# Kernel tuning notes

Measured on AMD Instinct MI355X. Metric: run time of the kernel, lower is better.

Reference implementation:

```python
import jax, jax.numpy as jnp
import numpy as np

B, S, D = 16, 8192, 512
H, K, V = 8, 64, 64
EPS = 1e-12  # tf.math.l2_normalize epsilon


def setup_inputs() -> dict:
    key = jax.random.key(0)
    ks = jax.random.split(key, 12)
    s = 0.02
    return {
        "x": jax.random.normal(ks[0], (B, S, D), jnp.float32),
        "mask": jnp.ones((B, S), dtype=bool),
        "Wq_r": jax.random.normal(ks[1], (H, D, K), jnp.float32) * s,
        "bq_r": jnp.zeros((H, K), jnp.float32),
        "Wq_i": jax.random.normal(ks[2], (H, D, K), jnp.float32) * s,
        "bq_i": jnp.zeros((H, K), jnp.float32),
        "Wv": jax.random.normal(ks[3], (H, D, V), jnp.float32) * s,
        "bv": jnp.zeros((H, V), jnp.float32),
        "key_real": jax.random.normal(ks[4], (H, K), jnp.float32),
        "key_imag": jax.random.normal(ks[5], (H, K), jnp.float32),
        "Wf": jax.random.normal(ks[6], (H * V, D), jnp.float32) * s,
        "bf": jnp.zeros((D,), jnp.float32),
    }


def reference(x, mask, Wq_r, bq_r, Wq_i, bq_i, Wv, bv, key_real, key_imag, Wf, bf):
    m = mask.astype(x.dtype)  # [B,S]
    # all heads' query (complex: real/imag) and value projections in batched GEMMs
    qr = jnp.einsum('bsd,hdk->bshk', x, Wq_r) + bq_r  # [B,S,H,K]
    qi = jnp.einsum('bsd,hdk->bshk', x, Wq_i) + bq_i
    v = jnp.einsum('bsd,hdv->bshv', x, Wv) + bv       # [B,S,H,V]
    # complex l2_normalize along last axis: z / sqrt(sum |z|^2)
    qn = jnp.sqrt(jnp.maximum(jnp.sum(qr * qr + qi * qi, -1, keepdims=True), EPS))
    qr, qi = qr / qn, qi / qn
    kn = jnp.sqrt(jnp.maximum(jnp.sum(key_real**2 + key_imag**2, -1, keepdims=True), EPS))
    kr, ki = key_real / kn, key_imag / kn             # [H,K]
    # real part of non-conjugated complex dot product (operation='real')
    score = jnp.einsum('bshk,hk->bsh', qr, kr) - jnp.einsum('bshk,hk->bsh', qi, ki)
    score = score * m[:, :, None]                     # [B,S,H]
    pooled = jnp.einsum('bsh,bshv->bhv', score, v)    # masked weighted sum over S
    res = pooled.reshape(pooled.shape[0], -1)          # concat heads -> [B,H*V]
    return res @ Wf + bf                               # feedforward -> [B,D]
```

## Files before the change

kernel.cpp:

```cpp
#include <hip/hip_runtime.h>
#include <hip/hip_bf16.h>


#define CB 16
#define CS 8192
#define CD 512
#define CH 8
#define CK 64
#define NCOL 128
#define TM 64
#define EPSV 1e-12f

typedef __attribute__((ext_vector_type(8))) unsigned short us8;
typedef __attribute__((ext_vector_type(8))) __bf16 bf16x8;
typedef __attribute__((ext_vector_type(4))) float f32x4;

__device__ __forceinline__ unsigned short f2bf(float f) {
  __hip_bfloat16 h = __float2bfloat16(f);
  return *reinterpret_cast<unsigned short*>(&h);
}
__device__ __forceinline__ float bf2f(unsigned short u) {
  unsigned int x = ((unsigned int)u) << 16;
  return __uint_as_float(x);
}
__device__ __forceinline__ bf16x8 as_bf(us8 u) { return __builtin_bit_cast(bf16x8, u); }

#define G2L16(gp, lp)                                                  \
  __builtin_amdgcn_global_load_lds(                                    \
      (const __attribute__((address_space(1))) unsigned int*)(gp),     \
      (__attribute__((address_space(3))) unsigned int*)(lp), 16, 0, 0)

__global__ void cap_prep(const float* __restrict__ Wq_r, const float* __restrict__ Wq_i,
                         unsigned short* __restrict__ wbt) {
  __shared__ float tile[64][65];
  int blk = blockIdx.x, t = threadIdx.x;
  int ri = blk >> 6, h = (blk >> 3) & 7, dt = blk & 7;
  const float* src = (ri ? Wq_i : Wq_r) + (size_t)h * CD * CK + (size_t)dt * 64 * CK;
  #pragma unroll
  for (int p = 0; p < 16; ++p) {
    int idx = p * 256 + t;
    int d = idx >> 6, c = idx & 63;
    tile[d][c] = src[(size_t)d * CK + c];
  }
  __syncthreads();
  int l = t & 63;
  #pragma unroll
  for (int p = 0; p < 16; ++p) {
    int c = p * 4 + (t >> 6);
    wbt[((size_t)(h * NCOL + ri * 64 + c)) * CD + dt * 64 + l] = f2bf(tile[l][c]);
  }
}

__global__ void cap_keys(const float* __restrict__ key_real, const float* __restrict__ key_imag,
                         const float* __restrict__ bq_r, const float* __restrict__ bq_i,
                         float* __restrict__ wvec, float* __restrict__ bqc) {
  int h = blockIdx.x, t = threadIdx.x;
  __shared__ float kn;
  if (t < 64) {
    float a = key_real[h * CK + t], b2 = key_imag[h * CK + t];
    float s = a * a + b2 * b2;
    #pragma unroll
    for (int off = 1; off < 64; off <<= 1) s += __shfl_xor(s, off);
    if (t == 0) kn = sqrtf(fmaxf(s, EPSV));
  }
  __syncthreads();
  float v = (t < CK) ? key_real[h * CK + t] : -key_imag[h * CK + (t - CK)];
  wvec[h * NCOL + t] = v / kn;
  bqc[h * NCOL + t] = (t < CK) ? bq_r[h * CK + t] : bq_i[h * CK + (t - CK)];
}

#define XL_BYTES 65536
#define WBUF_BYTES 32768
#define SMEM_BYTES (XL_BYTES + 2 * WBUF_BYTES + 3 * 2048)

__global__ __launch_bounds__(512, 2) void cap_main(
    const float* __restrict__ x, const int* __restrict__ mask,
    const unsigned short* __restrict__ wbt, const float* __restrict__ wvec,
    const float* __restrict__ bqc, float* __restrict__ yws, float* __restrict__ ssum) {
  extern __shared__ char smem[];
  char* Xl = smem;
  char* Wb = smem + XL_BYTES;
  float* partn = (float*)(smem + XL_BYTES + 2 * WBUF_BYTES);
  float* partm = partn + 512;
  float* scoresA = partm + 512;

  const int tid = threadIdx.x;
  const int w = tid >> 6, l = tid & 63;
  const int lr = l & 15, q = l >> 4;
  const int b = blockIdx.x >> 7;
  const int s0 = (blockIdx.x & 127) * TM;
  const float* xrow = x + ((size_t)(b * CS + s0)) * CD;

  auto stageW = [&](int s) {
    if (s >= 32) return;
    int ch = s >> 4, kc = s & 15;
    char* dst = Wb + (size_t)(s & 1) * WBUF_BYTES;
    #pragma unroll
    for (int i = 0; i < 4; ++i) {
      int o = i * 8192 + tid * 16;
      int col_local = o >> 6;
      int kchunk = (o >> 4) & 3;
      const unsigned short* src =
          wbt + ((size_t)(ch * 512 + col_local)) * CD + kc * 32 + kchunk * 8;
      G2L16(src, dst + o);
    }
  };

  stageW(0);

  #pragma unroll
  for (int i = 0; i < 8; ++i) {
    int id = i * 512 + tid;
    int row = id >> 6, cc = id & 63;
    const float* src = xrow + row * CD + cc * 8;
    float4 f0 = *(const float4*)(src);
    float4 f1 = *(const float4*)(src + 4);
    us8 v;
    v[0] = f2bf(f0.x); v[1] = f2bf(f0.y); v[2] = f2bf(f0.z); v[3] = f2bf(f0.w);
    v[4] = f2bf(f1.x); v[5] = f2bf(f1.y); v[6] = f2bf(f1.z); v[7] = f2bf(f1.w);
    int byte = row * 1024 + ((cc * 16) ^ ((row & 7) << 4));
    *(us8*)(Xl + byte) = v;
  }
  __syncthreads();

  #pragma unroll 1
  for (int ch = 0; ch < 2; ++ch) {
    f32x4 acc[4][4];
    #pragma unroll
    for (int m = 0; m < 4; ++m)
      #pragma unroll
      for (int n = 0; n < 4; ++n) acc[m][n] = (f32x4){0.f, 0.f, 0.f, 0.f};

    #pragma unroll 1
    for (int kc = 0; kc < 16; ++kc) {
      int gp = ch * 16 + kc;
      stageW(gp + 1);
      char* wl = Wb + (size_t)(gp & 1) * WBUF_BYTES;
      int kbyte = kc * 64 + q * 16;
      bf16x8 a[4], bb[4];
      #pragma unroll
      for (int m = 0; m < 4; ++m) {
        int row = m * 16 + lr;
        a[m] = as_bf(*(const us8*)(Xl + row * 1024 + (kbyte ^ ((row & 7) << 4))));
      }
      #pragma unroll
      for (int n = 0; n < 4; ++n) {
        int col_local = w * 64 + n * 16 + lr;
        bb[n] = as_bf(*(const us8*)(wl + col_local * 64 + q * 16));
      }
      #pragma unroll
      for (int m = 0; m < 4; ++m)
        #pragma unroll
        for (int n = 0; n < 4; ++n)
          acc[m][n] = __builtin_amdgcn_mfma_f32_16x16x32_bf16(a[m], bb[n], acc[m][n], 0, 0, 0);
      __syncthreads();
    }

    {
      int h = ch * 4 + (w >> 1);
      float n2[4][4], nm[4][4];
      #pragma unroll
      for (int m = 0; m < 4; ++m)
        #pragma unroll
        for (int r = 0; r < 4; ++r) { n2[m][r] = 0.f; nm[m][r] = 0.f; }
      #pragma unroll
      for (int n = 0; n < 4; ++n) {
        int c = (w & 1) * 64 + n * 16 + lr;
        float wv = wvec[h * NCOL + c];
        float bq = bqc[h * NCOL + c];
        #pragma unroll
        for (int m = 0; m < 4; ++m)
          #pragma unroll
          for (int r = 0; r < 4; ++r) {
            float qv = acc[m][n][r] + bq;
            n2[m][r] += qv * qv;
            nm[m][r] += qv * wv;
          }
      }
      #pragma unroll
      for (int off = 1; off < 16; off <<= 1)
        #pragma unroll
        for (int m = 0; m < 4; ++m)
          #pragma unroll
          for (int r = 0; r < 4; ++r) {
            n2[m][r] += __shfl_xor(n2[m][r], off);
            nm[m][r] += __shfl_xor(nm[m][r], off);
          }
      if (lr == 0) {
        #pragma unroll
        for (int m = 0; m < 4; ++m)
          #pragma unroll
          for (int r = 0; r < 4; ++r) {
            int row = m * 16 + q * 4 + r;
            partn[w * 64 + row] = n2[m][r];
            partm[w * 64 + row] = nm[m][r];
          }
      }
      __syncthreads();
      if (tid < 64) {
        float mk = (mask[(size_t)b * CS + s0 + tid] != 0) ? 1.0f : 0.0f;
        #pragma unroll
        for (int hl = 0; hl < 4; ++hl) {
          float nn = partn[(2 * hl) * 64 + tid] + partn[(2 * hl + 1) * 64 + tid];
          float mm = partm[(2 * hl) * 64 + tid] + partm[(2 * hl + 1) * 64 + tid];
          float sc = mm / sqrtf(fmaxf(nn, EPSV)) * mk;
          scoresA[(ch * 4 + hl) * 64 + tid] = sc;
          float ts = sc;
          #pragma unroll
          for (int off = 1; off < 64; off <<= 1) ts += __shfl_xor(ts, off);
          if (tid == 0) atomicAdd(&ssum[b * CH + ch * 4 + hl], ts);
        }
      }
      __syncthreads();
    }
  }

  {
    int d = tid;
    float sreg[CH];
    #pragma unroll
    for (int h = 0; h < CH; ++h) sreg[h] = scoresA[h * 64 + l];
    float yacc[CH];
    #pragma unroll
    for (int h = 0; h < CH; ++h) yacc[h] = 0.f;
    #pragma unroll 4
    for (int row = 0; row < TM; ++row) {
      int byte = row * 1024 + ((d * 2) ^ ((row & 7) << 4));
      float xv = bf2f(*(const unsigned short*)(Xl + byte));
      #pragma unroll
      for (int h = 0; h < CH; ++h) {
        float sc = __uint_as_float(
            __builtin_amdgcn_readlane(__float_as_uint(sreg[h]), row));
        yacc[h] += sc * xv;
      }
    }
    #pragma unroll
    for (int h = 0; h < CH; ++h)
      atomicAdd(&yws[((size_t)b * CH + h) * CD + d], yacc[h]);
  }
}

__global__ void cap_pooled(const float* __restrict__ yws, const float* __restrict__ ssum,
                           const float* __restrict__ Wv, const float* __restrict__ bv,
                           float* __restrict__ pooled) {
  int blk = blockIdx.x, t = threadIdx.x;
  int b = blk >> 3, h = blk & 7;
  int v = t & 63, dq = t >> 6;
  const float* y = yws + ((size_t)b * CH + h) * CD;
  const float* wv = Wv + (size_t)h * CD * CK;
  float acc = 0.f;
  #pragma unroll 8
  for (int i = 0; i < 128; ++i) {
    int d = i * 4 + dq;
    acc += y[d] * wv[(size_t)d * CK + v];
  }
  __shared__ float red[4][64];
  red[dq][v] = acc;
  __syncthreads();
  if (t < 64) {
    float s = red[0][t] + red[1][t] + red[2][t] + red[3][t] +
              ssum[b * CH + h] * bv[h * CK + t];
    pooled[(size_t)b * 512 + h * 64 + t] = s;
  }
}

__global__ void cap_out(const float* __restrict__ pooled, const float* __restrict__ Wf,
                        const float* __restrict__ bfv, float* __restrict__ out) {
  int blk = blockIdx.x, t = threadIdx.x;
  int b = blk >> 3, dc = blk & 7;
  int dl = t & 63, jq = t >> 6;
  int dout = dc * 64 + dl;
  const float* pr = pooled + (size_t)b * 512;
  float acc = 0.f;
  #pragma unroll 8
  for (int i = 0; i < 128; ++i) {
    int j = i * 4 + jq;
    acc += pr[j] * Wf[(size_t)j * CD + dout];
  }
  __shared__ float red[4][64];
  red[jq][dl] = acc;
  __syncthreads();
  if (t < 64)
    out[(size_t)b * CD + dc * 64 + t] =
        red[0][t] + red[1][t] + red[2][t] + red[3][t] + bfv[dc * 64 + t];
}

extern "C" void kernel_launch(void* const* d_in, const int* in_sizes, int n_in,
                              void* d_out, int out_size, void* d_ws, size_t ws_size,
                              hipStream_t stream) {
  const float* x = (const float*)d_in[0];
  const int* mask = (const int*)d_in[1];
  const float* Wq_r = (const float*)d_in[2];
  const float* bq_r = (const float*)d_in[3];
  const float* Wq_i = (const float*)d_in[4];
  const float* bq_i = (const float*)d_in[5];
  const float* Wv = (const float*)d_in[6];
  const float* bv = (const float*)d_in[7];
  const float* key_real = (const float*)d_in[8];
  const float* key_imag = (const float*)d_in[9];
  const float* Wf = (const float*)d_in[10];
  const float* bfv = (const float*)d_in[11];
  float* out = (float*)d_out;

  char* ws = (char*)d_ws;
  unsigned short* wbt = (unsigned short*)ws;
  float* wvec = (float*)(ws + (1 << 20));
  float* bqc  = (float*)(ws + (1 << 20) + 4096);
  float* yws  = (float*)(ws + (1 << 20) + 8192);
  float* ssum = (float*)(ws + (1 << 20) + 8192 + CB * CH * CD * 4);
  float* pooled = (float*)(ws + (1 << 20) + 8192 + CB * CH * CD * 4 + 512);

  hipMemsetAsync(yws, 0, CB * CH * CD * 4 + CB * CH * 4, stream);
  cap_prep<<<dim3(128), dim3(256), 0, stream>>>(Wq_r, Wq_i, wbt);
  cap_keys<<<dim3(8), dim3(128), 0, stream>>>(key_real, key_imag, bq_r, bq_i, wvec, bqc);
  hipFuncSetAttribute((const void*)cap_main,
                      hipFuncAttributeMaxDynamicSharedMemorySize, SMEM_BYTES);
  cap_main<<<dim3(CB * (CS / TM)), dim3(512), SMEM_BYTES, stream>>>(
      x, mask, wbt, wvec, bqc, yws, ssum);
  cap_pooled<<<dim3(128), dim3(256), 0, stream>>>(yws, ssum, Wv, bv, pooled);
  cap_out<<<dim3(128), dim3(256), 0, stream>>>(pooled, Wf, bfv, out);
}
```

Measured before the change: 735.1 us.

## Make main kernel persistent over tiles with register-streamed weights and fused epilogue

Each block of the main kernel now processes eight consecutive 64-row tiles instead of one, and the grid shrinks from 2048 to 256 blocks. Weight fragments are loaded straight from global memory into double-buffered registers instead of being staged through LDS. The next tile of x is prefetched into registers during the last k-chunk. Per-tile score-sum atomics and y atomics are accumulated in registers and flushed once per block, and the 16-lane reductions use DPP row rotates. The two tail kernels are merged into a single per-batch finish kernel. The changes aim to cut LDS staging, per-k barriers, atomics and launches, at the cost of higher register pressure, more global weight traffic through L2, and only 256 blocks to spread across the GPU.

```diff
diff --git a/kernel.cpp b/kernel.cpp
--- a/kernel.cpp
+++ b/kernel.cpp
@@ -9,6 +9,7 @@
 #define CK 64
 #define NCOL 128
 #define TM 64
+#define NT 8
 #define EPSV 1e-12f
 
 typedef __attribute__((ext_vector_type(8))) unsigned short us8;
@@ -25,10 +26,18 @@
 }
 __device__ __forceinline__ bf16x8 as_bf(us8 u) { return __builtin_bit_cast(bf16x8, u); }
 
-#define G2L16(gp, lp)                                                  \
-  __builtin_amdgcn_global_load_lds(                                    \
-      (const __attribute__((address_space(1))) unsigned int*)(gp),     \
-      (__attribute__((address_space(3))) unsigned int*)(lp), 16, 0, 0)
+__device__ __forceinline__ float ror_add16(float v) {
+  int x;
+  x = __builtin_amdgcn_update_dpp(0, __float_as_int(v), 0x128, 0xf, 0xf, false);
+  v += __int_as_float(x);
+  x = __builtin_amdgcn_update_dpp(0, __float_as_int(v), 0x124, 0xf, 0xf, false);
+  v += __int_as_float(x);
+  x = __builtin_amdgcn_update_dpp(0, __float_as_int(v), 0x122, 0xf, 0xf, false);
+  v += __int_as_float(x);
+  x = __builtin_amdgcn_update_dpp(0, __float_as_int(v), 0x121, 0xf, 0xf, false);
+  v += __int_as_float(x);
+  return v;
+}
 
 __global__ void cap_prep(const float* __restrict__ Wq_r, const float* __restrict__ Wq_i,
                          unsigned short* __restrict__ wbt) {
@@ -70,8 +79,7 @@
 }
 
 #define XL_BYTES 65536
-#define WBUF_BYTES 32768
-#define SMEM_BYTES (XL_BYTES + 2 * WBUF_BYTES + 3 * 2048)
+#define SMEM_BYTES (XL_BYTES + 3 * 512 * 4)
 
 __global__ __launch_bounds__(512, 2) void cap_main(
     const float* __restrict__ x, const int* __restrict__ mask,
@@ -79,113 +87,124 @@
     const float* __restrict__ bqc, float* __restrict__ yws, float* __restrict__ ssum) {
   extern __shared__ char smem[];
   char* Xl = smem;
-  char* Wb = smem + XL_BYTES;
-  float* partn = (float*)(smem + XL_BYTES + 2 * WBUF_BYTES);
+  float* scoresA = (float*)(smem + XL_BYTES);
+  float* partn = scoresA + 512;
   float* partm = partn + 512;
-  float* scoresA = partm + 512;
 
   const int tid = threadIdx.x;
   const int w = tid >> 6, l = tid & 63;
   const int lr = l & 15, q = l >> 4;
-  const int b = blockIdx.x >> 7;
-  const int s0 = (blockIdx.x & 127) * TM;
-  const float* xrow = x + ((size_t)(b * CS + s0)) * CD;
-
-  auto stageW = [&](int s) {
-    if (s >= 32) return;
-    int ch = s >> 4, kc = s & 15;
-    char* dst = Wb + (size_t)(s & 1) * WBUF_BYTES;
-    #pragma unroll
-    for (int i = 0; i < 4; ++i) {
-      int o = i * 8192 + tid * 16;
-      int col_local = o >> 6;
-      int kchunk = (o >> 4) & 3;
-      const unsigned short* src =
-          wbt + ((size_t)(ch * 512 + col_local)) * CD + kc * 32 + kchunk * 8;
-      G2L16(src, dst + o);
-    }
-  };
-
-  stageW(0);
+  const int b = blockIdx.x >> 4;
+  const int s_base = (blockIdx.x & 15) * (NT * TM);
+  const float* xbase = x + ((size_t)b * CS + s_base) * CD;
+  const us8* wbt8 = (const us8*)wbt;
+  const int hw = w >> 1, chalf = w & 1;
+
+  float yacc[CH], ssacc[CH];
+  #pragma unroll
+  for (int h = 0; h < CH; ++h) { yacc[h] = 0.f; ssacc[h] = 0.f; }
+
+  float4 xp[16];
 
   #pragma unroll
   for (int i = 0; i < 8; ++i) {
     int id = i * 512 + tid;
     int row = id >> 6, cc = id & 63;
-    const float* src = xrow + row * CD + cc * 8;
-    float4 f0 = *(const float4*)(src);
-    float4 f1 = *(const float4*)(src + 4);
+    const float* src = xbase + row * CD + cc * 8;
+    xp[i * 2] = *(const float4*)(src);
+    xp[i * 2 + 1] = *(const float4*)(src + 4);
+  }
+  #pragma unroll
+  for (int i = 0; i < 8; ++i) {
+    int id = i * 512 + tid;
+    int row = id >> 6, cc = id & 63;
+    float4 f0 = xp[i * 2], f1 = xp[i * 2 + 1];
     us8 v;
     v[0] = f2bf(f0.x); v[1] = f2bf(f0.y); v[2] = f2bf(f0.z); v[3] = f2bf(f0.w);
     v[4] = f2bf(f1.x); v[5] = f2bf(f1.y); v[6] = f2bf(f1.z); v[7] = f2bf(f1.w);
-    int byte = row * 1024 + ((cc * 16) ^ ((row & 7) << 4));
-    *(us8*)(Xl + byte) = v;
+    *(us8*)(Xl + row * 1024 + ((cc * 16) ^ ((row & 7) << 4))) = v;
   }
   __syncthreads();
 
   #pragma unroll 1
-  for (int ch = 0; ch < 2; ++ch) {
-    f32x4 acc[4][4];
+  for (int t = 0; t < NT; ++t) {
     #pragma unroll
-    for (int m = 0; m < 4; ++m)
-      #pragma unroll
-      for (int n = 0; n < 4; ++n) acc[m][n] = (f32x4){0.f, 0.f, 0.f, 0.f};
-
-    #pragma unroll 1
-    for (int kc = 0; kc < 16; ++kc) {
-      int gp = ch * 16 + kc;
-      stageW(gp + 1);
-      char* wl = Wb + (size_t)(gp & 1) * WBUF_BYTES;
-      int kbyte = kc * 64 + q * 16;
-      bf16x8 a[4], bb[4];
-      #pragma unroll
-      for (int m = 0; m < 4; ++m) {
-        int row = m * 16 + lr;
-        a[m] = as_bf(*(const us8*)(Xl + row * 1024 + (kbyte ^ ((row & 7) << 4))));
-      }
+    for (int ch = 0; ch < 2; ++ch) {
+      const int hh = ch * 4 + hw;
+      const us8* wB = wbt8 + (size_t)hh * 8192 + chalf * 4096 + lr * 64 + q;
+
+      f32x4 acc[4][4];
+      #pragma unroll
+      for (int m = 0; m < 4; ++m)
+        #pragma unroll
+        for (int n = 0; n < 4; ++n) acc[m][n] = (f32x4){0.f, 0.f, 0.f, 0.f};
+
+      us8 wbuf[2][4];
+      #pragma unroll
+      for (int n = 0; n < 4; ++n) wbuf[0][n] = wB[n * 1024];
+
+      #pragma unroll
+      for (int kc = 0; kc < 16; ++kc) {
+        if (kc < 15) {
+          #pragma unroll
+          for (int n = 0; n < 4; ++n)
+            wbuf[(kc + 1) & 1][n] = wB[n * 1024 + (kc + 1) * 4];
+        }
+        if (ch == 1 && kc == 15 && t < NT - 1) {
+          const float* xnext = xbase + (size_t)(t + 1) * TM * CD;
+          #pragma unroll
+          for (int i = 0; i < 8; ++i) {
+            int id = i * 512 + tid;
+            int row = id >> 6, cc = id & 63;
+            const float* src = xnext + row * CD + cc * 8;
+            xp[i * 2] = *(const float4*)(src);
+            xp[i * 2 + 1] = *(const float4*)(src + 4);
+          }
+        }
+        bf16x8 a[4];
+        #pragma unroll
+        for (int m = 0; m < 4; ++m) {
+          int row = m * 16 + lr;
+          a[m] = as_bf(*(const us8*)(Xl + row * 1024 +
+                                     ((kc * 64 + q * 16) ^ ((row & 7) << 4))));
+        }
+        #pragma unroll
+        for (int m = 0; m < 4; ++m)
+          #pragma unroll
+          for (int n = 0; n < 4; ++n)
+            acc[m][n] = __builtin_amdgcn_mfma_f32_16x16x32_bf16(
+                a[m], as_bf(wbuf[kc & 1][n]), acc[m][n], 0, 0, 0);
+      }
+
+      float wv_[4], bq_[4];
       #pragma unroll
       for (int n = 0; n < 4; ++n) {
-        int col_local = w * 64 + n * 16 + lr;
-        bb[n] = as_bf(*(const us8*)(wl + col_local * 64 + q * 16));
-      }
+        int c = hh * NCOL + chalf * 64 + n * 16 + lr;
+        wv_[n] = wvec[c];
+        bq_[n] = bqc[c];
+      }
+      float n2[4][4], nm[4][4];
       #pragma unroll
       for (int m = 0; m < 4; ++m)
         #pragma unroll
-        for (int n = 0; n < 4; ++n)
-          acc[m][n] = __builtin_amdgcn_mfma_f32_16x16x32_bf16(a[m], bb[n], acc[m][n], 0, 0, 0);
-      __syncthreads();
-    }
-
-    {
-      int h = ch * 4 + (w >> 1);
-      float n2[4][4], nm[4][4];
+        for (int r = 0; r < 4; ++r) { n2[m][r] = 0.f; nm[m][r] = 0.f; }
+      #pragma unroll
+      for (int n = 0; n < 4; ++n)
+        #pragma unroll
+        for (int m = 0; m < 4; ++m)
+          #pragma unroll
+          for (int r = 0; r < 4; ++r) {
+            float qv = acc[m][n][r] + bq_[n];
+            n2[m][r] += qv * qv;
+            nm[m][r] += qv * wv_[n];
+          }
       #pragma unroll
       for (int m = 0; m < 4; ++m)
         #pragma unroll
-        for (int r = 0; r < 4; ++r) { n2[m][r] = 0.f; nm[m][r] = 0.f; }
-      #pragma unroll
-      for (int n = 0; n < 4; ++n) {
-        int c = (w & 1) * 64 + n * 16 + lr;
-        float wv = wvec[h * NCOL + c];
-        float bq = bqc[h * NCOL + c];
-        #pragma unroll
-        for (int m = 0; m < 4; ++m)
-          #pragma unroll
-          for (int r = 0; r < 4; ++r) {
-            float qv = acc[m][n][r] + bq;
-            n2[m][r] += qv * qv;
-            nm[m][r] += qv * wv;
-          }
-      }
-      #pragma unroll
-      for (int off = 1; off < 16; off <<= 1)
-        #pragma unroll
-        for (int m = 0; m < 4; ++m)
-          #pragma unroll
-          for (int r = 0; r < 4; ++r) {
-            n2[m][r] += __shfl_xor(n2[m][r], off);
-            nm[m][r] += __shfl_xor(nm[m][r], off);
-          }
+        for (int r = 0; r < 4; ++r) {
+          n2[m][r] = ror_add16(n2[m][r]);
+          nm[m][r] = ror_add16(nm[m][r]);
+        }
       if (lr == 0) {
         #pragma unroll
         for (int m = 0; m < 4; ++m)
@@ -198,91 +217,95 @@
       }
       __syncthreads();
       if (tid < 64) {
-        float mk = (mask[(size_t)b * CS + s0 + tid] != 0) ? 1.0f : 0.0f;
+        float mk = (mask[(size_t)b * CS + s_base + t * TM + tid] != 0) ? 1.0f : 0.0f;
         #pragma unroll
         for (int hl = 0; hl < 4; ++hl) {
           float nn = partn[(2 * hl) * 64 + tid] + partn[(2 * hl + 1) * 64 + tid];
           float mm = partm[(2 * hl) * 64 + tid] + partm[(2 * hl + 1) * 64 + tid];
           float sc = mm / sqrtf(fmaxf(nn, EPSV)) * mk;
           scoresA[(ch * 4 + hl) * 64 + tid] = sc;
-          float ts = sc;
-          #pragma unroll
-          for (int off = 1; off < 64; off <<= 1) ts += __shfl_xor(ts, off);
-          if (tid == 0) atomicAdd(&ssum[b * CH + ch * 4 + hl], ts);
+          ssacc[ch * 4 + hl] += sc;
         }
       }
       __syncthreads();
     }
-  }
-
+
+    {
+      int d = tid;
+      float sreg[CH];
+      #pragma unroll
+      for (int h = 0; h < CH; ++h) sreg[h] = scoresA[h * 64 + l];
+      #pragma unroll 4
+      for (int row = 0; row < TM; ++row) {
+        float xv = bf2f(*(const unsigned short*)(
+            Xl + row * 1024 + ((d * 2) ^ ((row & 7) << 4))));
+        #pragma unroll
+        for (int h = 0; h < CH; ++h) {
+          float sc = __uint_as_float(
+              __builtin_amdgcn_readlane(__float_as_uint(sreg[h]), row));
+          yacc[h] += sc * xv;
+        }
+      }
+    }
+    __syncthreads();
+
+    if (t < NT - 1) {
+      #pragma unroll
+      for (int i = 0; i < 8; ++i) {
+        int id = i * 512 + tid;
+        int row = id >> 6, cc = id & 63;
+        float4 f0 = xp[i * 2], f1 = xp[i * 2 + 1];
+        us8 v;
+        v[0] = f2bf(f0.x); v[1] = f2bf(f0.y); v[2] = f2bf(f0.z); v[3] = f2bf(f0.w);
+        v[4] = f2bf(f1.x); v[5] = f2bf(f1.y); v[6] = f2bf(f1.z); v[7] = f2bf(f1.w);
+        *(us8*)(Xl + row * 1024 + ((cc * 16) ^ ((row & 7) << 4))) = v;
+      }
+      __syncthreads();
+    }
+  }
+
+  #pragma unroll
+  for (int h = 0; h < CH; ++h)
+    atomicAdd(&yws[((size_t)b * CH + h) * CD + tid], yacc[h]);
+  if (tid < 64) {
+    #pragma unroll
+    for (int h = 0; h < CH; ++h) {
+      float s = ssacc[h];
+      #pragma unroll
+      for (int off = 1; off < 64; off <<= 1) s += __shfl_xor(s, off);
+      if (l == 0) atomicAdd(&ssum[b * CH + h], s);
+    }
+  }
+}
+
+__global__ void cap_finish(const float* __restrict__ yws, const float* __restrict__ ssum,
+                           const float* __restrict__ Wv, const float* __restrict__ bv,
+                           const float* __restrict__ Wf, const float* __restrict__ bfv,
+                           float* __restrict__ out) {
+  __shared__ float yl[CH * CD];
+  __shared__ float pl[512];
+  __shared__ float ss[CH];
+  int b = blockIdx.x, t = threadIdx.x;
+  #pragma unroll
+  for (int i = 0; i < 8; ++i) yl[i * 512 + t] = yws[(size_t)b * CH * CD + i * 512 + t];
+  if (t < CH) ss[t] = ssum[b * CH + t];
+  __syncthreads();
   {
-    int d = tid;
-    float sreg[CH];
-    #pragma unroll
-    for (int h = 0; h < CH; ++h) sreg[h] = scoresA[h * 64 + l];
-    float yacc[CH];
-    #pragma unroll
-    for (int h = 0; h < CH; ++h) yacc[h] = 0.f;
-    #pragma unroll 4
-    for (int row = 0; row < TM; ++row) {
-      int byte = row * 1024 + ((d * 2) ^ ((row & 7) << 4));
-      float xv = bf2f(*(const unsigned short*)(Xl + byte));
-      #pragma unroll
-      for (int h = 0; h < CH; ++h) {
-        float sc = __uint_as_float(
-            __builtin_amdgcn_readlane(__float_as_uint(sreg[h]), row));
-        yacc[h] += sc * xv;
-      }
-    }
-    #pragma unroll
-    for (int h = 0; h < CH; ++h)
-      atomicAdd(&yws[((size_t)b * CH + h) * CD + d], yacc[h]);
-  }
-}
-
-__global__ void cap_pooled(const float* __restrict__ yws, const float* __restrict__ ssum,
-                           const float* __restrict__ Wv, const float* __restrict__ bv,
-                           float* __restrict__ pooled) {
-  int blk = blockIdx.x, t = threadIdx.x;
-  int b = blk >> 3, h = blk & 7;
-  int v = t & 63, dq = t >> 6;
-  const float* y = yws + ((size_t)b * CH + h) * CD;
-  const float* wv = Wv + (size_t)h * CD * CK;
-  float acc = 0.f;
-  #pragma unroll 8
-  for (int i = 0; i < 128; ++i) {
-    int d = i * 4 + dq;
-    acc += y[d] * wv[(size_t)d * CK + v];
-  }
-  __shared__ float red[4][64];
-  red[dq][v] = acc;
-  __syncthreads();
-  if (t < 64) {
-    float s = red[0][t] + red[1][t] + red[2][t] + red[3][t] +
-              ssum[b * CH + h] * bv[h * CK + t];
-    pooled[(size_t)b * 512 + h * 64 + t] = s;
-  }
-}
-
-__global__ void cap_out(const float* __restrict__ pooled, const float* __restrict__ Wf,
-                        const float* __restrict__ bfv, float* __restrict__ out) {
-  int blk = blockIdx.x, t = threadIdx.x;
-  int b = blk >> 3, dc = blk & 7;
-  int dl = t & 63, jq = t >> 6;
-  int dout = dc * 64 + dl;
-  const float* pr = pooled + (size_t)b * 512;
-  float acc = 0.f;
-  #pragma unroll 8
-  for (int i = 0; i < 128; ++i) {
-    int j = i * 4 + jq;
-    acc += pr[j] * Wf[(size_t)j * CD + dout];
-  }
-  __shared__ float red[4][64];
-  red[jq][dl] = acc;
-  __syncthreads();
-  if (t < 64)
-    out[(size_t)b * CD + dc * 64 + t] =
-        red[0][t] + red[1][t] + red[2][t] + red[3][t] + bfv[dc * 64 + t];
+    int h = t >> 6, v = t & 63;
+    float acc = ss[h] * bv[h * CK + v];
+    const float* yrow = yl + h * CD;
+    const float* wcol = Wv + (size_t)h * CD * CK + v;
+    #pragma unroll 8
+    for (int d = 0; d < CD; ++d) acc += yrow[d] * wcol[(size_t)d * CK];
+    pl[t] = acc;
+  }
+  __syncthreads();
+  {
+    float o = bfv[t];
+    #pragma unroll 8
+    for (int j = 0; j < 512; ++j) o += pl[j] * Wf[(size_t)j * CD + t];
+    out[(size_t)b * CD + t] = o;
+  }
 }
 
 extern "C" void kernel_launch(void* const* d_in, const int* in_sizes, int n_in,
@@ -308,15 +331,13 @@
   float* bqc  = (float*)(ws + (1 << 20) + 4096);
   float* yws  = (float*)(ws + (1 << 20) + 8192);
   float* ssum = (float*)(ws + (1 << 20) + 8192 + CB * CH * CD * 4);
-  float* pooled = (float*)(ws + (1 << 20) + 8192 + CB * CH * CD * 4 + 512);
 
   hipMemsetAsync(yws, 0, CB * CH * CD * 4 + CB * CH * 4, stream);
   cap_prep<<<dim3(128), dim3(256), 0, stream>>>(Wq_r, Wq_i, wbt);
   cap_keys<<<dim3(8), dim3(128), 0, stream>>>(key_real, key_imag, bq_r, bq_i, wvec, bqc);
   hipFuncSetAttribute((const void*)cap_main,
                       hipFuncAttributeMaxDynamicSharedMemorySize, SMEM_BYTES);
-  cap_main<<<dim3(CB * (CS / TM)), dim3(512), SMEM_BYTES, stream>>>(
+  cap_main<<<dim3(CB * 16), dim3(512), SMEM_BYTES, stream>>>(
       x, mask, wbt, wvec, bqc, yws, ssum);
-  cap_pooled<<<dim3(128), dim3(256), 0, stream>>>(yws, ssum, Wv, bv, pooled);
-  cap_out<<<dim3(128), dim3(256), 0, stream>>>(pooled, Wf, bfv, out);
-}
+  cap_finish<<<dim3(CB), dim3(512), 0, stream>>>(yws, ssum, Wv, bv, Wf, bfv, out);
+}
```

Result: slower. 1.153 ms (+56.8%).
